# Kernel tuning notes

Hardware: AMD Instinct MI355X
Metric: run time of the kernel (lower is better)

## Reference

```python
import jax, jax.numpy as jnp
import numpy as np

CROP_H, CROP_W = 14, 14
EXTRAPOLATION_VALUE = 0.0


def setup_inputs() -> dict:
    key = jax.random.key(0)
    k1, k2, k3 = jax.random.split(key, 3)
    image = jax.random.normal(k1, (8, 256, 200, 200), dtype=jnp.float32)
    boxes = jax.random.uniform(k2, (1000, 4), dtype=jnp.float32)  # (y1, x1, y2, x2) normalized
    box_indices = jax.random.randint(k3, (1000,), 0, 8, dtype=jnp.int32)
    return {"image": image, "boxes": boxes, "box_indices": box_indices}


def _gather_corners(image, box_indices, y_idx, x_idx):
    # image: [N, C, H, W]; y_idx: [B, ch]; x_idx: [B, cw] -> [B, C, ch, cw]
    g = image[box_indices[:, None, None], :, y_idx[:, :, None], x_idx[:, None, :]]  # [B, ch, cw, C]
    return jnp.transpose(g, (0, 3, 1, 2))


def _crop_and_resize(image, boxes, box_indices):
    N, C, H, W = image.shape
    y1, x1, y2, x2 = boxes[:, 0], boxes[:, 1], boxes[:, 2], boxes[:, 3]  # [B]

    h_scale = (y2 - y1) * (H - 1) / (CROP_H - 1)  # [B]
    w_scale = (x2 - x1) * (W - 1) / (CROP_W - 1)

    t_y = jnp.arange(CROP_H, dtype=boxes.dtype)
    t_x = jnp.arange(CROP_W, dtype=boxes.dtype)
    in_y = y1[:, None] * (H - 1) + t_y[None, :] * h_scale[:, None]  # [B, ch]
    in_x = x1[:, None] * (W - 1) + t_x[None, :] * w_scale[:, None]  # [B, cw]

    # extrapolation masks (True = out of range)
    mask_y = (in_y > H - 1) | (in_y < 0)  # [B, ch]
    mask_x = (in_x > W - 1) | (in_x < 0)  # [B, cw]
    valid = ~(mask_y[:, :, None] | mask_x[:, None, :])  # [B, ch, cw]
    in_y = jnp.where(mask_y, 0.0, in_y)
    in_x = jnp.where(mask_x, 0.0, in_x)

    top_y = jnp.floor(in_y).astype(jnp.int32)   # [B, ch]
    bot_y = jnp.ceil(in_y).astype(jnp.int32)
    left_x = jnp.floor(in_x).astype(jnp.int32)  # [B, cw]
    right_x = jnp.ceil(in_x).astype(jnp.int32)
    y_lerp = in_y - top_y.astype(in_y.dtype)    # [B, ch]
    x_lerp = in_x - left_x.astype(in_x.dtype)   # [B, cw]

    tl = _gather_corners(image, box_indices, top_y, left_x)   # [B, C, ch, cw]
    tr = _gather_corners(image, box_indices, top_y, right_x)
    bl = _gather_corners(image, box_indices, bot_y, left_x)
    br = _gather_corners(image, box_indices, bot_y, right_x)

    xl = x_lerp[:, None, None, :]  # broadcast over C, ch
    top = tl + xl * (tr - tl)
    bottom = bl + xl * (br - bl)
    crop = top + y_lerp[:, None, :, None] * (bottom - top)  # [B, C, ch, cw]

    m = valid.astype(image.dtype)[:, None, :, :]  # [B, 1, ch, cw]
    return crop * m + (1.0 - m) * EXTRAPOLATION_VALUE


def reference(image, boxes, box_indices):
    return _crop_and_resize(image, boxes, box_indices)
```

## Files before the change

kernel.cpp:

```cpp
#include <hip/hip_runtime.h>

#define CROP_H 14
#define CROP_W 14
#define IMG_H 200
#define IMG_W 200
#define IMG_C 256
#define N_IMG 8
#define N_BOXES 1000
#define PLANE (IMG_H * IMG_W)
#define ELEMS_PER_BOX (IMG_C * CROP_H * CROP_W)
#define BLOCKS_PER_BOX (ELEMS_PER_BOX / 256)

__global__ __launch_bounds__(512) void prep_kernel(
    const float* __restrict__ boxes, const int* __restrict__ box_idx,
    int* __restrict__ order, float* __restrict__ ytab, float* __restrict__ xtab)
{
    __shared__ int counts[N_IMG];
    __shared__ int offsets[N_IMG];
    int tid  = threadIdx.x;
    int wave = tid >> 6;
    int lane = tid & 63;

    int cnt = 0;
    for (int i = lane; i < N_BOXES; i += 64) cnt += (box_idx[i] == wave) ? 1 : 0;
    for (int off = 32; off; off >>= 1) cnt += __shfl_down(cnt, off);
    if (lane == 0) counts[wave] = cnt;
    __syncthreads();
    if (tid == 0) {
        int s = 0;
        for (int i = 0; i < N_IMG; i++) { offsets[i] = s; s += counts[i]; }
    }
    __syncthreads();

    int base = offsets[wave];
    for (int i0 = 0; i0 < N_BOXES; i0 += 64) {
        int i = i0 + lane;
        bool p = (i < N_BOXES) && (box_idx[i] == wave);
        unsigned long long m = __ballot(p);
        unsigned long long below = m & ((1ull << lane) - 1ull);
        if (p) order[base + __popcll(below)] = i;
        base += __popcll(m);
    }

    for (int i = tid; i < N_BOXES * CROP_H; i += 512) {
        int b = i / CROP_H;
        int t = i % CROP_H;
        float y1 = boxes[b * 4 + 0];
        float x1 = boxes[b * 4 + 1];
        float y2 = boxes[b * 4 + 2];
        float x2 = boxes[b * 4 + 3];
        float h_scale = (y2 - y1) * (float)(IMG_H - 1) / (float)(CROP_H - 1);
        float w_scale = (x2 - x1) * (float)(IMG_W - 1) / (float)(CROP_W - 1);
        float vy = y1 * (float)(IMG_H - 1) + (float)t * h_scale;
        float vx = x1 * (float)(IMG_W - 1) + (float)t * w_scale;
        ytab[i] = ((vy > (float)(IMG_H - 1)) || (vy < 0.0f)) ? -1.0f : vy;
        xtab[i] = ((vx > (float)(IMG_W - 1)) || (vx < 0.0f)) ? -1.0f : vx;
    }
}

__global__ __launch_bounds__(256) void crop_resize_kernel(
    const float* __restrict__ image,
    const int*   __restrict__ box_idx,
    const int*   __restrict__ order,
    const float* __restrict__ ytab,
    const float* __restrict__ xtab,
    float*       __restrict__ out)
{
    int pos    = blockIdx.x % N_BOXES;
    int within = blockIdx.x / N_BOXES;
    int b      = order[pos];
    int elem   = within * 256 + threadIdx.x;

    int x = elem % CROP_W;
    int t = elem / CROP_W;
    int y = t % CROP_H;
    int c = t / CROP_H;

    float vy = ytab[b * CROP_H + y];
    float vx = xtab[b * CROP_H + x];

    size_t oidx = (size_t)b * ELEMS_PER_BOX + elem;

    if ((vy < 0.0f) || (vx < 0.0f)) {
        __builtin_nontemporal_store(0.0f, &out[oidx]);
        return;
    }

    int ty = (int)floorf(vy);
    int by = (int)ceilf(vy);
    int lx = (int)floorf(vx);
    int rx = (int)ceilf(vx);
    float yl = vy - (float)ty;
    float xl = vx - (float)lx;

    int n = box_idx[b];
    const float* __restrict__ plane =
        image + ((size_t)n * IMG_C + c) * (size_t)PLANE;

    int basex = min(lx, IMG_W - 2);
    const float* pt = plane + ty * IMG_W + basex;
    const float* pb = plane + by * IMG_W + basex;

    float2 vt, vbo;
    __builtin_memcpy(&vt,  pt, sizeof(float2));
    __builtin_memcpy(&vbo, pb, sizeof(float2));

    float tl = (lx > basex) ? vt.y  : vt.x;
    float tr = vt.y;
    float bl = (lx > basex) ? vbo.y : vbo.x;
    float br = vbo.y;
    if (rx == lx) { tr = tl; br = bl; }

    float top = tl + xl * (tr - tl);
    float bot = bl + xl * (br - bl);
    float v   = top + yl * (bot - top);
    __builtin_nontemporal_store(v, &out[oidx]);
}

extern "C" void kernel_launch(void* const* d_in, const int* in_sizes, int n_in,
                              void* d_out, int out_size, void* d_ws, size_t ws_size,
                              hipStream_t stream) {
    const float* image   = (const float*)d_in[0];
    const float* boxes   = (const float*)d_in[1];
    const int*   box_idx = (const int*)d_in[2];
    float* out  = (float*)d_out;

    int*   order = (int*)d_ws;
    float* ytab  = (float*)((char*)d_ws + 4096);
    float* xtab  = ytab + N_BOXES * CROP_H;

    prep_kernel<<<1, 512, 0, stream>>>(boxes, box_idx, order, ytab, xtab);

    int grid = N_BOXES * BLOCKS_PER_BOX;
    crop_resize_kernel<<<grid, 256, 0, stream>>>(image, box_idx, order, ytab, xtab, out);
}
```

Before: 277.0 us.

## Stage needed image rows per box-channel in LDS before bilinear interpolation

```diff
diff --git a/kernel.cpp b/kernel.cpp
--- a/kernel.cpp
+++ b/kernel.cpp
@@ -8,12 +8,15 @@
 #define N_IMG 8
 #define N_BOXES 1000
 #define PLANE (IMG_H * IMG_W)
-#define ELEMS_PER_BOX (IMG_C * CROP_H * CROP_W)
-#define BLOCKS_PER_BOX (ELEMS_PER_BOX / 256)
+#define IMG_TOTAL (N_IMG * IMG_C * PLANE)
+#define HW (CROP_H * CROP_W)
+#define NSLOT (2 * CROP_H)
+#define BUF_STRIDE 204
 
 __global__ __launch_bounds__(512) void prep_kernel(
     const float* __restrict__ boxes, const int* __restrict__ box_idx,
-    int* __restrict__ order, float* __restrict__ ytab, float* __restrict__ xtab)
+    int* __restrict__ order, float* __restrict__ ytab, float* __restrict__ xtab,
+    int4* __restrict__ bmeta)
 {
     __shared__ int counts[N_IMG];
     __shared__ int offsets[N_IMG];
@@ -51,10 +54,27 @@
         float x2 = boxes[b * 4 + 3];
         float h_scale = (y2 - y1) * (float)(IMG_H - 1) / (float)(CROP_H - 1);
         float w_scale = (x2 - x1) * (float)(IMG_W - 1) / (float)(CROP_W - 1);
-        float vy = y1 * (float)(IMG_H - 1) + (float)t * h_scale;
-        float vx = x1 * (float)(IMG_W - 1) + (float)t * w_scale;
-        ytab[i] = ((vy > (float)(IMG_H - 1)) || (vy < 0.0f)) ? -1.0f : vy;
-        xtab[i] = ((vx > (float)(IMG_W - 1)) || (vx < 0.0f)) ? -1.0f : vx;
+        ytab[i] = y1 * (float)(IMG_H - 1) + (float)t * h_scale;
+        xtab[i] = x1 * (float)(IMG_W - 1) + (float)t * w_scale;
+    }
+
+    for (int b = tid; b < N_BOXES; b += 512) {
+        float x1 = boxes[b * 4 + 1];
+        float x2 = boxes[b * 4 + 3];
+        float w_scale = (x2 - x1) * (float)(IMG_W - 1) / (float)(CROP_W - 1);
+        int lxmin = IMG_W, rxmax = 0;
+        for (int t = 0; t < CROP_W; t++) {
+            float vx = x1 * (float)(IMG_W - 1) + (float)t * w_scale;
+            if ((vx > (float)(IMG_W - 1)) || (vx < 0.0f)) vx = 0.0f;
+            int lx = (int)floorf(vx);
+            int rx = (int)ceilf(vx);
+            lxmin = min(lxmin, lx);
+            rxmax = max(rxmax, rx);
+        }
+        int xmin4 = lxmin & ~3;
+        int rl4   = (rxmax - xmin4 + 1 + 3) >> 2;
+        float rcp = 1.0f / (float)rl4;
+        bmeta[b] = make_int4(xmin4, rl4, __float_as_int(rcp), 0);
     }
 }
 
@@ -64,57 +84,81 @@
     const int*   __restrict__ order,
     const float* __restrict__ ytab,
     const float* __restrict__ xtab,
+    const int4*  __restrict__ bmeta,
     float*       __restrict__ out)
 {
-    int pos    = blockIdx.x % N_BOXES;
-    int within = blockIdx.x / N_BOXES;
-    int b      = order[pos];
-    int elem   = within * 256 + threadIdx.x;
+    __shared__ int   s_slotrow[NSLOT];
+    __shared__ float s_yl[CROP_H];
+    __shared__ int   s_ymask[CROP_H];
+    __shared__ int   s_kl[CROP_W], s_kr[CROP_W];
+    __shared__ float s_xl[CROP_W];
+    __shared__ int   s_xmask[CROP_W];
+    __shared__ __align__(16) float buf[NSLOT][BUF_STRIDE];
 
-    int x = elem % CROP_W;
-    int t = elem / CROP_W;
-    int y = t % CROP_H;
-    int c = t / CROP_H;
+    int tid = threadIdx.x;
+    int pos = blockIdx.x % N_BOXES;
+    int c   = blockIdx.x / N_BOXES;
+    int b   = order[pos];
+    int n   = box_idx[b];
 
-    float vy = ytab[b * CROP_H + y];
-    float vx = xtab[b * CROP_H + x];
+    int4 meta  = bmeta[b];
+    int  xmin4 = meta.x;
+    int  rl4   = meta.y;
+    float rcp  = __int_as_float(meta.z);
 
-    size_t oidx = (size_t)b * ELEMS_PER_BOX + elem;
+    if (tid < CROP_H) {
+        float vy = ytab[b * CROP_H + tid];
+        int m = (vy > (float)(IMG_H - 1)) || (vy < 0.0f);
+        if (m) vy = 0.0f;
+        int ty = (int)floorf(vy);
+        int by = (int)ceilf(vy);
+        s_slotrow[2 * tid]     = ty;
+        s_slotrow[2 * tid + 1] = by;
+        s_yl[tid]    = vy - (float)ty;
+        s_ymask[tid] = m;
+    } else if (tid >= 64 && tid < 64 + CROP_W) {
+        int x = tid - 64;
+        float vx = xtab[b * CROP_H + x];
+        int m = (vx > (float)(IMG_W - 1)) || (vx < 0.0f);
+        if (m) vx = 0.0f;
+        int lx = (int)floorf(vx);
+        int rx = (int)ceilf(vx);
+        s_kl[x]    = lx - xmin4;
+        s_kr[x]    = rx - xmin4;
+        s_xl[x]    = vx - (float)lx;
+        s_xmask[x] = m;
+    }
+    __syncthreads();
 
-    if ((vy < 0.0f) || (vx < 0.0f)) {
-        __builtin_nontemporal_store(0.0f, &out[oidx]);
-        return;
+    unsigned plane_off = ((unsigned)n * IMG_C + c) * (unsigned)PLANE;
+    int total4 = NSLOT * rl4;
+    for (int i = tid; i < total4; i += 256) {
+        int r   = (int)(((float)i + 0.5f) * rcp);
+        int off = i - r * rl4;
+        unsigned goff = plane_off + (unsigned)(s_slotrow[r] * IMG_W + xmin4 + off * 4);
+        goff = min(goff, (unsigned)(IMG_TOTAL - 4));
+        float4 v = *(const float4*)(image + goff);
+        *(float4*)&buf[r][off * 4] = v;
     }
+    __syncthreads();
 
-    int ty = (int)floorf(vy);
-    int by = (int)ceilf(vy);
-    int lx = (int)floorf(vx);
-    int rx = (int)ceilf(vx);
-    float yl = vy - (float)ty;
-    float xl = vx - (float)lx;
-
-    int n = box_idx[b];
-    const float* __restrict__ plane =
-        image + ((size_t)n * IMG_C + c) * (size_t)PLANE;
-
-    int basex = min(lx, IMG_W - 2);
-    const float* pt = plane + ty * IMG_W + basex;
-    const float* pb = plane + by * IMG_W + basex;
-
-    float2 vt, vbo;
-    __builtin_memcpy(&vt,  pt, sizeof(float2));
-    __builtin_memcpy(&vbo, pb, sizeof(float2));
-
-    float tl = (lx > basex) ? vt.y  : vt.x;
-    float tr = vt.y;
-    float bl = (lx > basex) ? vbo.y : vbo.x;
-    float br = vbo.y;
-    if (rx == lx) { tr = tl; br = bl; }
-
-    float top = tl + xl * (tr - tl);
-    float bot = bl + xl * (br - bl);
-    float v   = top + yl * (bot - top);
-    __builtin_nontemporal_store(v, &out[oidx]);
+    if (tid < HW) {
+        int y = tid / CROP_W;
+        int x = tid % CROP_W;
+        int kl = s_kl[x], kr = s_kr[x];
+        float xl = s_xl[x];
+        float yl = s_yl[y];
+        float tl = buf[2 * y][kl];
+        float tr = buf[2 * y][kr];
+        float bl = buf[2 * y + 1][kl];
+        float br = buf[2 * y + 1][kr];
+        float top = tl + xl * (tr - tl);
+        float bot = bl + xl * (br - bl);
+        float v   = top + yl * (bot - top);
+        if (s_ymask[y] | s_xmask[x]) v = 0.0f;
+        size_t oidx = ((size_t)b * IMG_C + c) * (size_t)HW + tid;
+        __builtin_nontemporal_store(v, &out[oidx]);
+    }
 }
 
 extern "C" void kernel_launch(void* const* d_in, const int* in_sizes, int n_in,
@@ -128,9 +172,11 @@
     int*   order = (int*)d_ws;
     float* ytab  = (float*)((char*)d_ws + 4096);
     float* xtab  = ytab + N_BOXES * CROP_H;
+    int4*  bmeta = (int4*)((char*)d_ws + 116096);
 
-    prep_kernel<<<1, 512, 0, stream>>>(boxes, box_idx, order, ytab, xtab);
+    prep_kernel<<<1, 512, 0, stream>>>(boxes, box_idx, order, ytab, xtab, bmeta);
 
-    int grid = N_BOXES * BLOCKS_PER_BOX;
-    crop_resize_kernel<<<grid, 256, 0, stream>>>(image, box_idx, order, ytab, xtab, out);
+    int grid = N_BOXES * IMG_C;
+    crop_resize_kernel<<<grid, 256, 0, stream>>>(image, box_idx, order,
+                                                 ytab, xtab, bmeta, out);
 }
```

New measurement: 446.2 us. 61.1% more time.

## Map one block per box-channel with XCD-aware channel interleaving

Applied to the files above, without the earlier changes.

```diff
diff --git a/kernel.cpp b/kernel.cpp
--- a/kernel.cpp
+++ b/kernel.cpp
@@ -8,8 +8,7 @@
 #define N_IMG 8
 #define N_BOXES 1000
 #define PLANE (IMG_H * IMG_W)
-#define ELEMS_PER_BOX (IMG_C * CROP_H * CROP_W)
-#define BLOCKS_PER_BOX (ELEMS_PER_BOX / 256)
+#define HW (CROP_H * CROP_W)
 
 __global__ __launch_bounds__(512) void prep_kernel(
     const float* __restrict__ boxes, const int* __restrict__ box_idx,
@@ -51,10 +50,8 @@
         float x2 = boxes[b * 4 + 3];
         float h_scale = (y2 - y1) * (float)(IMG_H - 1) / (float)(CROP_H - 1);
         float w_scale = (x2 - x1) * (float)(IMG_W - 1) / (float)(CROP_W - 1);
-        float vy = y1 * (float)(IMG_H - 1) + (float)t * h_scale;
-        float vx = x1 * (float)(IMG_W - 1) + (float)t * w_scale;
-        ytab[i] = ((vy > (float)(IMG_H - 1)) || (vy < 0.0f)) ? -1.0f : vy;
-        xtab[i] = ((vx > (float)(IMG_W - 1)) || (vx < 0.0f)) ? -1.0f : vx;
+        ytab[i] = y1 * (float)(IMG_H - 1) + (float)t * h_scale;
+        xtab[i] = x1 * (float)(IMG_W - 1) + (float)t * w_scale;
     }
 }
 
@@ -66,25 +63,29 @@
     const float* __restrict__ xtab,
     float*       __restrict__ out)
 {
-    int pos    = blockIdx.x % N_BOXES;
-    int within = blockIdx.x / N_BOXES;
-    int b      = order[pos];
-    int elem   = within * 256 + threadIdx.x;
+    int tid = threadIdx.x;
+    if (tid >= HW) return;
 
-    int x = elem % CROP_W;
-    int t = elem / CROP_W;
-    int y = t % CROP_H;
-    int c = t / CROP_H;
+    int xcd = blockIdx.x & 7;
+    int j   = blockIdx.x >> 3;
+    int pos = j % N_BOXES;
+    int chi = j / N_BOXES;
+    int c   = chi * 8 + xcd;
+
+    int b = order[pos];
+    int n = box_idx[b];
+
+    int y = tid / CROP_W;
+    int x = tid % CROP_W;
 
     float vy = ytab[b * CROP_H + y];
     float vx = xtab[b * CROP_H + x];
 
-    size_t oidx = (size_t)b * ELEMS_PER_BOX + elem;
+    size_t oidx = ((size_t)b * IMG_C + c) * (size_t)HW + tid;
 
-    if ((vy < 0.0f) || (vx < 0.0f)) {
-        __builtin_nontemporal_store(0.0f, &out[oidx]);
-        return;
-    }
+    bool bad = (vy > (float)(IMG_H - 1)) || (vy < 0.0f) ||
+               (vx > (float)(IMG_W - 1)) || (vx < 0.0f);
+    if (bad) { __builtin_nontemporal_store(0.0f, &out[oidx]); return; }
 
     int ty = (int)floorf(vy);
     int by = (int)ceilf(vy);
@@ -93,23 +94,13 @@
     float yl = vy - (float)ty;
     float xl = vx - (float)lx;
 
-    int n = box_idx[b];
     const float* __restrict__ plane =
         image + ((size_t)n * IMG_C + c) * (size_t)PLANE;
 
-    int basex = min(lx, IMG_W - 2);
-    const float* pt = plane + ty * IMG_W + basex;
-    const float* pb = plane + by * IMG_W + basex;
-
-    float2 vt, vbo;
-    __builtin_memcpy(&vt,  pt, sizeof(float2));
-    __builtin_memcpy(&vbo, pb, sizeof(float2));
-
-    float tl = (lx > basex) ? vt.y  : vt.x;
-    float tr = vt.y;
-    float bl = (lx > basex) ? vbo.y : vbo.x;
-    float br = vbo.y;
-    if (rx == lx) { tr = tl; br = bl; }
+    float tl = plane[ty * IMG_W + lx];
+    float tr = plane[ty * IMG_W + rx];
+    float bl = plane[by * IMG_W + lx];
+    float br = plane[by * IMG_W + rx];
 
     float top = tl + xl * (tr - tl);
     float bot = bl + xl * (br - bl);
@@ -131,6 +122,7 @@
 
     prep_kernel<<<1, 512, 0, stream>>>(boxes, box_idx, order, ytab, xtab);
 
-    int grid = N_BOXES * BLOCKS_PER_BOX;
-    crop_resize_kernel<<<grid, 256, 0, stream>>>(image, box_idx, order, ytab, xtab, out);
+    int grid = N_BOXES * IMG_C;
+    crop_resize_kernel<<<grid, 256, 0, stream>>>(image, box_idx, order,
+                                                 ytab, xtab, out);
 }
```

Result: slower. 329.2 us (+18.8%).
